# Performance work log

Measured on AMD Instinct MI355X. Metric: run time of the kernel, lower is better.

Reference implementation:

```python
import jax, jax.numpy as jnp
import numpy as np
from jax import lax

H = 512; MEL = 80; B = 8; S = 128; T = 200; NCH = 256


def _lstm_layer(x, Wih, Whh, bih, bhh, reverse=False):
    # x: [B, S, Din] -> [B, S, H]; PyTorch gate order i,f,g,o
    xs = jnp.swapaxes(x, 0, 1)
    bsz = x.shape[0]
    hid = Whh.shape[1]

    def step(carry, xt):
        h, c = carry
        g = xt @ Wih.T + bih + h @ Whh.T + bhh
        i, f, gg, o = jnp.split(g, 4, axis=-1)
        c2 = jax.nn.sigmoid(f) * c + jax.nn.sigmoid(i) * jnp.tanh(gg)
        h2 = jax.nn.sigmoid(o) * jnp.tanh(c2)
        return (h2, c2), h2

    init = (jnp.zeros((bsz, hid), x.dtype), jnp.zeros((bsz, hid), x.dtype))
    _, hs = lax.scan(step, init, xs, reverse=reverse)
    return jnp.swapaxes(hs, 0, 1)


def _forward(text_sequence, target_mel_len, emb, Wih00, Whh00, bih00, bhh00,
             Wih01, Whh01, bih01, bhh01, Wih10, Whh10, bih10, bhh10,
             Wih11, Whh11, bih11, bhh11, attn_W, attn_b, attn_v,
             dec_Wih, dec_Whh, dec_bih, dec_bhh, mel_W, mel_b):
    x = emb[text_sequence]  # [B,S,H] (dropout disabled: eval mode)
    f0 = _lstm_layer(x, Wih00, Whh00, bih00, bhh00)
    b0 = _lstm_layer(x, Wih01, Whh01, bih01, bhh01, reverse=True)
    x1 = jnp.concatenate([f0, b0], axis=-1)
    f1 = _lstm_layer(x1, Wih10, Whh10, bih10, bhh10)
    b1 = _lstm_layer(x1, Wih11, Whh11, bih11, bhh11, reverse=True)
    enc = jnp.concatenate([f1, b1], axis=-1)  # [B,S,2H]

    # attn Linear on cat(hidden, encoder): split weight into hidden/encoder parts
    W_h = attn_W[:, :H]
    W_e = attn_W[:, H:]
    enc_part = jnp.einsum('bsd,hd->bsh', enc, W_e) + attn_b  # hoisted out of loop
    bsz = text_sequence.shape[0]

    def step(carry, _):
        h, c, din = carry
        energy = jnp.tanh(enc_part + (h @ W_h.T)[:, None, :])  # [B,S,H]
        score = energy @ attn_v                                # [B,S]
        a = jax.nn.softmax(score, axis=1)
        ctx = jnp.einsum('bs,bsd->bd', a, enc)                 # [B,2H]
        xin = jnp.concatenate([din, ctx], axis=1)              # [B,MEL+2H]
        g = xin @ dec_Wih.T + dec_bih + h @ dec_Whh.T + dec_bhh
        i, f, gg, o = jnp.split(g, 4, axis=-1)
        c2 = jax.nn.sigmoid(f) * c + jax.nn.sigmoid(i) * jnp.tanh(gg)
        h2 = jax.nn.sigmoid(o) * jnp.tanh(c2)
        mel = h2 @ mel_W.T + mel_b                             # [B,MEL]
        return (h2, c2, mel), mel

    carry0 = (jnp.zeros((bsz, H), jnp.float32),
              jnp.zeros((bsz, H), jnp.float32),
              jnp.zeros((bsz, MEL), jnp.float32))
    _, mels = lax.scan(step, carry0, None, length=target_mel_len)
    return jnp.transpose(mels, (1, 2, 0))  # [B, MEL, T]


def setup_inputs() -> dict:
    key = jax.random.key(0)
    keys = jax.random.split(key, 64)
    ki = iter(range(64))

    def rn(shape, scale=0.05):
        return jax.random.normal(keys[next(ki)], shape, dtype=jnp.float32) * scale

    inp = {}
    inp['text_sequence'] = jax.random.randint(keys[next(ki)], (B, S), 0, NCH)
    inp['target_mel_len'] = T
    inp['emb'] = rn((NCH, H), 0.3)
    for l, din in ((0, H), (1, 2 * H)):
        for d in (0, 1):
            inp[f'Wih{l}{d}'] = rn((4 * H, din))
            inp[f'Whh{l}{d}'] = rn((4 * H, H))
            inp[f'bih{l}{d}'] = rn((4 * H,))
            inp[f'bhh{l}{d}'] = rn((4 * H,))
    inp['attn_W'] = rn((H, 3 * H))
    inp['attn_b'] = rn((H,))
    inp['attn_v'] = rn((H,))
    inp['dec_Wih'] = rn((4 * H, 2 * H + MEL))
    inp['dec_Whh'] = rn((4 * H, H))
    inp['dec_bih'] = rn((4 * H,))
    inp['dec_bhh'] = rn((4 * H,))
    inp['mel_W'] = rn((MEL, H))
    inp['mel_b'] = rn((MEL,))
    return inp


def reference(text_sequence, target_mel_len, emb, Wih00, Whh00, bih00, bhh00,
              Wih01, Whh01, bih01, bhh01, Wih10, Whh10, bih10, bhh10,
              Wih11, Whh11, bih11, bhh11, attn_W, attn_b, attn_v,
              dec_Wih, dec_Whh, dec_bih, dec_bhh, mel_W, mel_b):
    return _forward(text_sequence, target_mel_len, emb, Wih00, Whh00, bih00, bhh00,
                    Wih01, Whh01, bih01, bhh01, Wih10, Whh10, bih10, bhh10,
                    Wih11, Whh11, bih11, bhh11, attn_W, attn_b, attn_v,
                    dec_Wih, dec_Whh, dec_bih, dec_bhh, mel_W, mel_b)
```

## Files before the change

### kernel.cpp

```cpp
#include <hip/hip_runtime.h>

#define B_ 8
#define S_ 128
#define H_ 512
#define G_ 2048
#define MEL_ 80

#define FLG_DEC    0
#define FLG_L0     8192
#define FLG_L1     10240
#define OFF_H0S    12288
#define OFF_H1S    28672
#define OFF_DH     45056
#define OFF_ATT    53248
#define OFF_HW     54272
#define ZERO_WORDS 58368
#define OFF_X0     58368
#define OFF_GX0F   (OFF_X0 + 524288)
#define OFF_GX0B   (OFF_GX0F + 2097152)
#define OFF_H0     (OFF_GX0B + 2097152)
#define OFF_GX1F   (OFF_H0 + 1048576)
#define OFF_GX1B   (OFF_GX1F + 2097152)
#define OFF_ENC    (OFF_GX1B + 2097152)
#define OFF_ENCP   (OFF_ENC + 1048576)
#define OFF_WE     OFF_GX0F
#define OFF_WH2    OFF_GX0B
#define OFF_BA     (OFF_GX0B + 1048576)
#define OFF_BB     (OFF_GX0B + 1050624)

__device__ __forceinline__ float sigm_f(float x) {
    x = fminf(fmaxf(x, -30.f), 30.f);
    return 1.f / (1.f + __expf(-x));
}
__device__ __forceinline__ float tanh_f(float x) {
    x = fminf(fmaxf(x, -15.f), 15.f);
    float e = __expf(2.f * x);
    return (e - 1.f) / (e + 1.f);
}

__device__ __forceinline__ void agw_u(unsigned* p, unsigned v) {
    __hip_atomic_store(p, v, __ATOMIC_RELAXED, __HIP_MEMORY_SCOPE_AGENT);
}
__device__ __forceinline__ unsigned agr_u(const unsigned* p) {
    return __hip_atomic_load(p, __ATOMIC_RELAXED, __HIP_MEMORY_SCOPE_AGENT);
}
__device__ __forceinline__ void agw_f(float* p, float v) {
    agw_u((unsigned*)p, __float_as_uint(v));
}
__device__ __forceinline__ float agr_f(const float* p) {
    return __uint_as_float(agr_u((const unsigned*)p));
}

__device__ __forceinline__ float4 agr_f4(const float* p) {
    float4 v;
    asm volatile("global_load_dwordx4 %0, %1, off sc1\n\t"
                 "s_waitcnt vmcnt(0)"
                 : "=v"(v) : "v"(p) : "memory");
    return v;
}

__device__ __forceinline__ void poll_flags(const unsigned* flags, int nf, unsigned phase) {
    if ((int)threadIdx.x < nf) {
        while (agr_u(flags + threadIdx.x * 16) < phase)
            __builtin_amdgcn_s_sleep(1);
    }
    __syncthreads();
}

__device__ __forceinline__ void set_flag(unsigned* flag, unsigned phase) {
    asm volatile("s_waitcnt vmcnt(0) lgkmcnt(0)" ::: "memory");
    __syncthreads();
    if (threadIdx.x == 0)
        agw_u(flag, phase);
}

__global__ __launch_bounds__(256) void zero_kernel(float* p) {
    p[blockIdx.x * 256 + threadIdx.x] = 0.f;
}

__global__ __launch_bounds__(256) void embed_kernel(const int* __restrict__ text,
                                                    const float* __restrict__ emb,
                                                    float* __restrict__ X) {
    int i = blockIdx.x * 256 + threadIdx.x;
    int bs = i >> 7;
    int h4 = i & 127;
    int ch = text[bs];
    ((float4*)X)[i] = ((const float4*)emb)[ch * 128 + h4];
}

__global__ __launch_bounds__(256) void gemm_f32(const float* __restrict__ A, int lda,
                                                const float* __restrict__ W, int ldw,
                                                const float* __restrict__ b1,
                                                const float* __restrict__ b2,
                                                float* __restrict__ C, int ldc, int K) {
    __shared__ float As[32][68];
    __shared__ float Ws[32][68];
    int tid = threadIdx.x;
    int tx = tid & 15, ty = tid >> 4;
    int n0 = blockIdx.x * 64, m0 = blockIdx.y * 64;
    float acc[4][4] = {};
    int r  = tid >> 3;
    int c4 = (tid & 7) * 4;
    for (int k0 = 0; k0 < K; k0 += 32) {
        float4 a0 = *(const float4*)&A[(m0 + r) * lda + k0 + c4];
        float4 a1 = *(const float4*)&A[(m0 + r + 32) * lda + k0 + c4];
        float4 w0 = *(const float4*)&W[(n0 + r) * ldw + k0 + c4];
        float4 w1 = *(const float4*)&W[(n0 + r + 32) * ldw + k0 + c4];
        As[c4 + 0][r] = a0.x; As[c4 + 1][r] = a0.y; As[c4 + 2][r] = a0.z; As[c4 + 3][r] = a0.w;
        As[c4 + 0][r + 32] = a1.x; As[c4 + 1][r + 32] = a1.y; As[c4 + 2][r + 32] = a1.z; As[c4 + 3][r + 32] = a1.w;
        Ws[c4 + 0][r] = w0.x; Ws[c4 + 1][r] = w0.y; Ws[c4 + 2][r] = w0.z; Ws[c4 + 3][r] = w0.w;
        Ws[c4 + 0][r + 32] = w1.x; Ws[c4 + 1][r + 32] = w1.y; Ws[c4 + 2][r + 32] = w1.z; Ws[c4 + 3][r + 32] = w1.w;
        __syncthreads();
#pragma unroll 8
        for (int kk = 0; kk < 32; ++kk) {
            float4 av = *(const float4*)&As[kk][ty * 4];
            float4 wv = *(const float4*)&Ws[kk][tx * 4];
            acc[0][0] = fmaf(av.x, wv.x, acc[0][0]); acc[0][1] = fmaf(av.x, wv.y, acc[0][1]);
            acc[0][2] = fmaf(av.x, wv.z, acc[0][2]); acc[0][3] = fmaf(av.x, wv.w, acc[0][3]);
            acc[1][0] = fmaf(av.y, wv.x, acc[1][0]); acc[1][1] = fmaf(av.y, wv.y, acc[1][1]);
            acc[1][2] = fmaf(av.y, wv.z, acc[1][2]); acc[1][3] = fmaf(av.y, wv.w, acc[1][3]);
            acc[2][0] = fmaf(av.z, wv.x, acc[2][0]); acc[2][1] = fmaf(av.z, wv.y, acc[2][1]);
            acc[2][2] = fmaf(av.z, wv.z, acc[2][2]); acc[2][3] = fmaf(av.z, wv.w, acc[2][3]);
            acc[3][0] = fmaf(av.w, wv.x, acc[3][0]); acc[3][1] = fmaf(av.w, wv.y, acc[3][1]);
            acc[3][2] = fmaf(av.w, wv.z, acc[3][2]); acc[3][3] = fmaf(av.w, wv.w, acc[3][3]);
        }
        __syncthreads();
    }
#pragma unroll
    for (int i = 0; i < 4; ++i)
#pragma unroll
        for (int j = 0; j < 4; ++j) {
            int n = n0 + tx * 4 + j;
            int m = m0 + ty * 4 + i;
            float bias = (b1 ? b1[n] : 0.f) + (b2 ? b2[n] : 0.f);
            C[m * ldc + n] = acc[i][j] + bias;
        }
}

__global__ __launch_bounds__(256) void we_kernel(const float* __restrict__ Wih,
                                                 const float* __restrict__ ENC,
                                                 float* __restrict__ WE) {
    const float* A = Wih + 80;
    const float* W = ENC + (size_t)blockIdx.z * 131072;
    float* C = WE + (size_t)blockIdx.z * 262144;
    __shared__ float As[32][68];
    __shared__ float Ws[32][68];
    int tid = threadIdx.x;
    int tx = tid & 15, ty = tid >> 4;
    int n0 = blockIdx.x * 64, m0 = blockIdx.y * 64;
    float acc[4][4] = {};
    int r  = tid >> 3;
    int c4 = (tid & 7) * 4;
    for (int k0 = 0; k0 < 1024; k0 += 32) {
        float4 a0 = *(const float4*)&A[(size_t)(m0 + r) * 1104 + k0 + c4];
        float4 a1 = *(const float4*)&A[(size_t)(m0 + r + 32) * 1104 + k0 + c4];
        float4 w0 = *(const float4*)&W[(n0 + r) * 1024 + k0 + c4];
        float4 w1 = *(const float4*)&W[(n0 + r + 32) * 1024 + k0 + c4];
        As[c4 + 0][r] = a0.x; As[c4 + 1][r] = a0.y; As[c4 + 2][r] = a0.z; As[c4 + 3][r] = a0.w;
        As[c4 + 0][r + 32] = a1.x; As[c4 + 1][r + 32] = a1.y; As[c4 + 2][r + 32] = a1.z; As[c4 + 3][r + 32] = a1.w;
        Ws[c4 + 0][r] = w0.x; Ws[c4 + 1][r] = w0.y; Ws[c4 + 2][r] = w0.z; Ws[c4 + 3][r] = w0.w;
        Ws[c4 + 0][r + 32] = w1.x; Ws[c4 + 1][r + 32] = w1.y; Ws[c4 + 2][r + 32] = w1.z; Ws[c4 + 3][r + 32] = w1.w;
        __syncthreads();
#pragma unroll 8
        for (int kk = 0; kk < 32; ++kk) {
            float4 av = *(const float4*)&As[kk][ty * 4];
            float4 wv = *(const float4*)&Ws[kk][tx * 4];
            acc[0][0] = fmaf(av.x, wv.x, acc[0][0]); acc[0][1] = fmaf(av.x, wv.y, acc[0][1]);
            acc[0][2] = fmaf(av.x, wv.z, acc[0][2]); acc[0][3] = fmaf(av.x, wv.w, acc[0][3]);
            acc[1][0] = fmaf(av.y, wv.x, acc[1][0]); acc[1][1] = fmaf(av.y, wv.y, acc[1][1]);
            acc[1][2] = fmaf(av.y, wv.z, acc[1][2]); acc[1][3] = fmaf(av.y, wv.w, acc[1][3]);
            acc[2][0] = fmaf(av.z, wv.x, acc[2][0]); acc[2][1] = fmaf(av.z, wv.y, acc[2][1]);
            acc[2][2] = fmaf(av.z, wv.z, acc[2][2]); acc[2][3] = fmaf(av.z, wv.w, acc[2][3]);
            acc[3][0] = fmaf(av.w, wv.x, acc[3][0]); acc[3][1] = fmaf(av.w, wv.y, acc[3][1]);
            acc[3][2] = fmaf(av.w, wv.z, acc[3][2]); acc[3][3] = fmaf(av.w, wv.w, acc[3][3]);
        }
        __syncthreads();
    }
#pragma unroll
    for (int i = 0; i < 4; ++i)
#pragma unroll
        for (int j = 0; j < 4; ++j)
            C[(size_t)(m0 + ty * 4 + i) * 128 + n0 + tx * 4 + j] = acc[i][j];
}

__global__ __launch_bounds__(256) void wh2_kernel(const float* __restrict__ Wih,
                                                  const float* __restrict__ Whh,
                                                  const float* __restrict__ melW,
                                                  float* __restrict__ WH2) {
    int wg = blockIdx.x;
    int tid = threadIdx.x;
    int r = wg >> 1;
    int k = (wg & 1) * 256 + tid;
    __shared__ float wrow[80];
    if (tid < 80) wrow[tid] = Wih[(size_t)r * 1104 + tid];
    __syncthreads();
    float acc = Whh[(size_t)r * 512 + k];
#pragma unroll 8
    for (int m = 0; m < 80; ++m)
        acc = fmaf(wrow[m], melW[m * 512 + k], acc);
    WH2[(size_t)r * 512 + k] = acc;
}

__global__ __launch_bounds__(256) void bias_kernel(const float* __restrict__ Wih,
                                                   const float* __restrict__ bih,
                                                   const float* __restrict__ bhh,
                                                   const float* __restrict__ melb,
                                                   float* __restrict__ BA,
                                                   float* __restrict__ BB) {
    int r = blockIdx.x * 256 + threadIdx.x;
    float a = bih[r] + bhh[r];
    float b2 = 0.f;
#pragma unroll 8
    for (int m = 0; m < 80; ++m)
        b2 = fmaf(Wih[(size_t)r * 1104 + m], melb[m], b2);
    BA[r] = a;
    BB[r] = a + b2;
}

__global__ __launch_bounds__(256) void lstm_kernel(const float* __restrict__ GXf,
                                                   const float* __restrict__ GXb,
                                                   const float* __restrict__ Whh_f,
                                                   const float* __restrict__ Whh_b,
                                                   float* __restrict__ Hout,
                                                   float* __restrict__ hstate,
                                                   unsigned* __restrict__ flagsL) {
    int wg  = blockIdx.x;
    int s   = wg & 7;
    int g16 = wg >> 3;
    int dir = g16 >> 3;
    int b   = g16 & 7;
    const float* GX  = dir ? GXb : GXf;
    const float* Whh = dir ? Whh_b : Whh_f;
    float* hs = hstate + g16 * 1024;
    unsigned* fg = flagsL + g16 * 128;

    int tid = threadIdx.x;
    int g = tid >> 6, c = tid & 63;
    int col = s * 64 + c;
    int grow = g * 512 + col;
    const float* wr = Whh + (size_t)grow * 512;

    __shared__ float hsh[512];
    __shared__ float gvL[4][64];

    float cst = 0.f;

    for (int t = 0; t < 128; ++t) {
        poll_flags(fg, 8, (unsigned)t);
        if (tid < 128) {
            float4 v = agr_f4(hs + (t & 1) * 512 + tid * 4);
            *(float4*)&hsh[tid * 4] = v;
        }
        __syncthreads();

        int st = dir ? (127 - t) : t;
        float acc = GX[((size_t)b * S_ + st) * G_ + grow];
        float a0 = 0.f, a1 = 0.f, a2 = 0.f, a3 = 0.f;
#pragma unroll 8
        for (int k = 0; k < 512; k += 4) {
            float4 wv = *(const float4*)(wr + k);
            float4 hv = *(const float4*)&hsh[k];
            a0 = fmaf(wv.x, hv.x, a0); a1 = fmaf(wv.y, hv.y, a1);
            a2 = fmaf(wv.z, hv.z, a2); a3 = fmaf(wv.w, hv.w, a3);
        }
        gvL[g][c] = acc + (a0 + a1) + (a2 + a3);
        __syncthreads();

        float h2 = 0.f;
        if (tid < 64) {
            float gi = gvL[0][tid], gf = gvL[1][tid];
            float gg = gvL[2][tid], go = gvL[3][tid];
            float c2 = sigm_f(gf) * cst + sigm_f(gi) * tanh_f(gg);
            h2 = sigm_f(go) * tanh_f(c2);
            cst = c2;
            agw_f(hs + ((t & 1) ^ 1) * 512 + s * 64 + tid, h2);
        }
        set_flag(fg + s * 16, (unsigned)(t + 1));
        if (tid < 64)
            Hout[((size_t)b * S_ + st) * 1024 + dir * 512 + s * 64 + tid] = h2;
    }
}

__global__ __launch_bounds__(256) void decoder_kernel(float* __restrict__ ws,
                                                      const float* __restrict__ attn_W,
                                                      const float* __restrict__ attn_v,
                                                      const float* __restrict__ mel_W,
                                                      const float* __restrict__ mel_b,
                                                      float* __restrict__ out, int T,
                                                      unsigned* __restrict__ flags) {
    float* ENCP = ws + OFF_ENCP;
    float* DH   = ws + OFF_DH;
    float* ATT  = ws + OFF_ATT;
    float* HW   = ws + OFF_HW;
    const float* WE  = ws + OFF_WE;
    const float* WH2 = ws + OFF_WH2;
    const float* BA  = ws + OFF_BA;
    const float* BB  = ws + OFF_BB;

    int wg  = blockIdx.x;
    int tid = threadIdx.x;

    if (wg < 128) {
        int s = wg & 15;
        int b = wg >> 4;
        unsigned* fC = flags + b * 1024;
        unsigned* fA = fC + 16 * 16;
        unsigned* fB = fC + 32 * 16;

        int r   = tid >> 1;
        int half = tid & 1;
        int grow = (r >> 5) * 512 + s * 32 + (r & 31);
        const float* wh2_half = WH2 + (size_t)grow * 512 + half * 256;
        const float* we_row   = WE + ((size_t)b * 2048 + grow) * 128 + half * 64;
        float bias_a = (half == 0) ? BA[grow] : 0.f;
        float bias_b = (half == 0) ? BB[grow] : 0.f;
        int r2 = tid & 31, oct = tid >> 5;
        const float* wh_row = attn_W + (size_t)(s * 32 + r2) * 1536 + oct * 64;

        __shared__ float hsh[512];
        __shared__ float hwred[32][9];
        __shared__ float gBx[128][2];
        __shared__ float gv[128];
        __shared__ float attL[128];

        float cst = 0.f;

        for (int t = 0; t < T; ++t) {
            poll_flags(fC, 16, (unsigned)t);
            const float* DHr = DH + (t & 1) * 4096 + b * 512;
            if (tid < 128) {
                float4 v = agr_f4(DHr + tid * 4);
                *(float4*)&hsh[tid * 4] = v;
            }
            __syncthreads();
            {
                const float* hp = hsh + oct * 64;
                float w = 0.f;
#pragma unroll 8
                for (int k = 0; k < 64; k += 4) {
                    float4 wv = *(const float4*)(wh_row + k);
                    float4 hv = *(const float4*)(hp + k);
                    w = fmaf(wv.x, hv.x, w); w = fmaf(wv.y, hv.y, w);
                    w = fmaf(wv.z, hv.z, w); w = fmaf(wv.w, hv.w, w);
                }
                hwred[r2][oct] = w;
            }
            __syncthreads();
            if (tid < 32) {
                float hw = hwred[tid][0] + hwred[tid][1] + hwred[tid][2] + hwred[tid][3]
                         + hwred[tid][4] + hwred[tid][5] + hwred[tid][6] + hwred[tid][7];
                agw_f(HW + b * 512 + s * 32 + tid, hw);
            }
            set_flag(fA + s * 16, (unsigned)(t + 1));

            float wpart = (t == 0) ? bias_a : bias_b;
            {
                const float* hp = hsh + half * 256;
                float a0 = 0.f, a1 = 0.f, a2 = 0.f, a3 = 0.f;
#pragma unroll 8
                for (int k = 0; k < 256; k += 4) {
                    float4 wv = *(const float4*)(wh2_half + k);
                    float4 hv = *(const float4*)(hp + k);
                    a0 = fmaf(wv.x, hv.x, a0); a1 = fmaf(wv.y, hv.y, a1);
                    a2 = fmaf(wv.z, hv.z, a2); a3 = fmaf(wv.w, hv.w, a3);
                }
                wpart += (a0 + a1) + (a2 + a3);
            }

            poll_flags(fB, 1, (unsigned)(t + 1));
            if (tid < 32) {
                float4 v = agr_f4(ATT + b * 128 + tid * 4);
                *(float4*)&attL[tid * 4] = v;
            }
            __syncthreads();
            {
                const float* ap = attL + half * 64;
                float a0 = 0.f, a1 = 0.f, a2 = 0.f, a3 = 0.f;
#pragma unroll 8
                for (int k = 0; k < 64; k += 4) {
                    float4 wv = *(const float4*)(we_row + k);
                    a0 = fmaf(wv.x, ap[k + 0], a0); a1 = fmaf(wv.y, ap[k + 1], a1);
                    a2 = fmaf(wv.z, ap[k + 2], a2); a3 = fmaf(wv.w, ap[k + 3], a3);
                }
                gBx[r][half] = wpart + (a0 + a1) + (a2 + a3);
            }
            __syncthreads();
            if (tid < 128)
                gv[tid] = gBx[tid][0] + gBx[tid][1];
            __syncthreads();
            if (tid < 32) {
                float gi = gv[tid], gf = gv[32 + tid], gg = gv[64 + tid], go = gv[96 + tid];
                float c2 = sigm_f(gf) * cst + sigm_f(gi) * tanh_f(gg);
                float h2 = sigm_f(go) * tanh_f(c2);
                cst = c2;
                agw_f(DH + ((t + 1) & 1) * 4096 + b * 512 + s * 32 + tid, h2);
            }
            set_flag(fC + s * 16, (unsigned)(t + 1));
        }
    } else {
        int b = wg - 128;
        unsigned* fC = flags + b * 1024;
        unsigned* fA = fC + 16 * 16;
        unsigned* fB = fC + 32 * 16;

        __shared__ float hw2[512];
        __shared__ float dh2[512];
        __shared__ float scred[128][2];
        __shared__ float red[128];
        __shared__ float att[128];
        __shared__ float melp[80][2];

        int r = tid >> 1, half = tid & 1;

        for (int t = 0; t < T; ++t) {
            poll_flags(fA, 16, (unsigned)(t + 1));
            if (tid < 128) {
                float4 v = agr_f4(HW + b * 512 + tid * 4);
                *(float4*)&hw2[tid * 4] = v;
            }
            __syncthreads();

            {
                int sI = tid & 127, kh = tid >> 7;
                const float* ep = ENCP + ((size_t)b * S_ + sI) * 512 + kh * 256;
                const float* hp = hw2 + kh * 256;
                const float* vv = attn_v + kh * 256;
                float a0 = 0.f, a1 = 0.f, a2 = 0.f, a3 = 0.f;
#pragma unroll 4
                for (int k = 0; k < 256; k += 4) {
                    float4 e4 = *(const float4*)(ep + k);
                    float4 h4 = *(const float4*)(hp + k);
                    float4 v4 = *(const float4*)(vv + k);
                    a0 = fmaf(tanh_f(e4.x + h4.x), v4.x, a0);
                    a1 = fmaf(tanh_f(e4.y + h4.y), v4.y, a1);
                    a2 = fmaf(tanh_f(e4.z + h4.z), v4.z, a2);
                    a3 = fmaf(tanh_f(e4.w + h4.w), v4.w, a3);
                }
                scred[sI][kh] = (a0 + a1) + (a2 + a3);
            }
            __syncthreads();

            float sc = 0.f;
            if (tid < 128) {
                sc = scred[tid][0] + scred[tid][1];
                red[tid] = sc;
            }
            __syncthreads();
            for (int off = 64; off >= 1; off >>= 1) {
                if (tid < off) red[tid] = fmaxf(red[tid], red[tid + off]);
                __syncthreads();
            }
            float mx = red[0];
            __syncthreads();
            if (tid < 128) {
                float e = __expf(sc - mx);
                att[tid] = e;
                red[tid] = e;
            }
            __syncthreads();
            if (tid < 64) red[tid] += red[tid + 64];
            __syncthreads();
            for (int off = 32; off >= 1; off >>= 1) {
                if (tid < off) red[tid] += red[tid + off];
                __syncthreads();
            }
            float inv = 1.f / red[0];
            if (tid < 128)
                agw_f(ATT + b * 128 + tid, att[tid] * inv);
            set_flag(fB, (unsigned)(t + 1));

            if (t > 0) {
                if (tid < 128) {
                    float4 v = agr_f4(DH + (t & 1) * 4096 + b * 512 + tid * 4);
                    *(float4*)&dh2[tid * 4] = v;
                }
                __syncthreads();
                if (tid < 160) {
                    const float* wp = mel_W + (size_t)r * 512 + half * 256;
                    const float* hp = dh2 + half * 256;
                    float a0 = 0.f, a1 = 0.f, a2 = 0.f, a3 = 0.f;
#pragma unroll 8
                    for (int k = 0; k < 256; k += 4) {
                        float4 wv = *(const float4*)(wp + k);
                        float4 hv = *(const float4*)(hp + k);
                        a0 = fmaf(wv.x, hv.x, a0); a1 = fmaf(wv.y, hv.y, a1);
                        a2 = fmaf(wv.z, hv.z, a2); a3 = fmaf(wv.w, hv.w, a3);
                    }
                    melp[r][half] = (a0 + a1) + (a2 + a3);
                }
                __syncthreads();
                if (tid < 80)
                    out[b * MEL_ * T + tid * T + (t - 1)] = melp[tid][0] + melp[tid][1] + mel_b[tid];
            }
        }

        poll_flags(fC, 16, (unsigned)T);
        if (tid < 128) {
            float4 v = agr_f4(DH + (T & 1) * 4096 + b * 512 + tid * 4);
            *(float4*)&dh2[tid * 4] = v;
        }
        __syncthreads();
        if (tid < 160) {
            const float* wp = mel_W + (size_t)r * 512 + half * 256;
            const float* hp = dh2 + half * 256;
            float a0 = 0.f, a1 = 0.f, a2 = 0.f, a3 = 0.f;
#pragma unroll 8
            for (int k = 0; k < 256; k += 4) {
                float4 wv = *(const float4*)(wp + k);
                float4 hv = *(const float4*)(hp + k);
                a0 = fmaf(wv.x, hv.x, a0); a1 = fmaf(wv.y, hv.y, a1);
                a2 = fmaf(wv.z, hv.z, a2); a3 = fmaf(wv.w, hv.w, a3);
            }
            melp[r][half] = (a0 + a1) + (a2 + a3);
        }
        __syncthreads();
        if (tid < 80)
            out[b * MEL_ * T + tid * T + (T - 1)] = melp[tid][0] + melp[tid][1] + mel_b[tid];
    }
}

extern "C" void kernel_launch(void* const* d_in, const int* in_sizes, int n_in,
                              void* d_out, int out_size, void* d_ws, size_t ws_size,
                              hipStream_t stream) {
    const int*   text  = (const int*)d_in[0];
    const float* emb   = (const float*)d_in[2];
    const float* Wih00 = (const float*)d_in[3];
    const float* Whh00 = (const float*)d_in[4];
    const float* bih00 = (const float*)d_in[5];
    const float* bhh00 = (const float*)d_in[6];
    const float* Wih01 = (const float*)d_in[7];
    const float* Whh01 = (const float*)d_in[8];
    const float* bih01 = (const float*)d_in[9];
    const float* bhh01 = (const float*)d_in[10];
    const float* Wih10 = (const float*)d_in[11];
    const float* Whh10 = (const float*)d_in[12];
    const float* bih10 = (const float*)d_in[13];
    const float* bhh10 = (const float*)d_in[14];
    const float* Wih11 = (const float*)d_in[15];
    const float* Whh11 = (const float*)d_in[16];
    const float* bih11 = (const float*)d_in[17];
    const float* bhh11 = (const float*)d_in[18];
    const float* attn_W = (const float*)d_in[19];
    const float* attn_b = (const float*)d_in[20];
    const float* attn_v = (const float*)d_in[21];
    const float* dec_Wih = (const float*)d_in[22];
    const float* dec_Whh = (const float*)d_in[23];
    const float* dec_bih = (const float*)d_in[24];
    const float* dec_bhh = (const float*)d_in[25];
    const float* mel_W = (const float*)d_in[26];
    const float* mel_b = (const float*)d_in[27];

    float* ws = (float*)d_ws;
    unsigned* flags = (unsigned*)d_ws;
    float* out = (float*)d_out;
    int T = out_size / (B_ * MEL_);

    zero_kernel<<<ZERO_WORDS / 256, 256, 0, stream>>>(ws);

    embed_kernel<<<512, 256, 0, stream>>>(text, emb, ws + OFF_X0);

    gemm_f32<<<dim3(32, 16), 256, 0, stream>>>(ws + OFF_X0, 512, Wih00, 512,
                                               bih00, bhh00, ws + OFF_GX0F, 2048, 512);
    gemm_f32<<<dim3(32, 16), 256, 0, stream>>>(ws + OFF_X0, 512, Wih01, 512,
                                               bih01, bhh01, ws + OFF_GX0B, 2048, 512);
    lstm_kernel<<<128, 256, 0, stream>>>(ws + OFF_GX0F, ws + OFF_GX0B, Whh00, Whh01,
                                         ws + OFF_H0, ws + OFF_H0S, flags + FLG_L0);
    wh2_kernel<<<4096, 256, 0, stream>>>(dec_Wih, dec_Whh, mel_W, ws + OFF_WH2);
    bias_kernel<<<8, 256, 0, stream>>>(dec_Wih, dec_bih, dec_bhh, mel_b,
                                       ws + OFF_BA, ws + OFF_BB);
    gemm_f32<<<dim3(32, 16), 256, 0, stream>>>(ws + OFF_H0, 1024, Wih10, 1024,
                                               bih10, bhh10, ws + OFF_GX1F, 2048, 1024);
    gemm_f32<<<dim3(32, 16), 256, 0, stream>>>(ws + OFF_H0, 1024, Wih11, 1024,
                                               bih11, bhh11, ws + OFF_GX1B, 2048, 1024);
    lstm_kernel<<<128, 256, 0, stream>>>(ws + OFF_GX1F, ws + OFF_GX1B, Whh10, Whh11,
                                         ws + OFF_ENC, ws + OFF_H1S, flags + FLG_L1);
    gemm_f32<<<dim3(8, 16), 256, 0, stream>>>(ws + OFF_ENC, 1024, attn_W + 512, 1536,
                                              attn_b, nullptr, ws + OFF_ENCP, 512, 1024);
    we_kernel<<<dim3(2, 32, 8), 256, 0, stream>>>(dec_Wih, ws + OFF_ENC, ws + OFF_WE);
    decoder_kernel<<<136, 256, 0, stream>>>(ws, attn_W, attn_v, mel_W, mel_b, out, T,
                                            flags + FLG_DEC);
}
```

Baseline: 9.865 ms.

## Restructure decoder sync: move hidden-attention projection into attention block, fewer workgroups

The h@W_h projection moves out of the 128 gate workgroups and into the per-batch attention workgroup. This removes one cross-workgroup flag handshake (fA/HW) per decoder step. The gate workgroups drop from 128 to 64, each now computing a full 512-long dot product per gate row instead of two halves, with fewer reductions and barriers. Flag polling is also merged with the hidden-state loads in both the LSTM and decoder kernels, and only the writing wave waits before setting the flag, instead of a block-wide barrier. The trade-off is more serial work per step in the attention workgroup and less parallelism overall.

New measurement: 16.12 ms. +63.4%, slower.

```diff
diff --git a/kernel.cpp b/kernel.cpp
--- a/kernel.cpp
+++ b/kernel.cpp
@@ -47,9 +47,6 @@
 __device__ __forceinline__ void agw_f(float* p, float v) {
     agw_u((unsigned*)p, __float_as_uint(v));
 }
-__device__ __forceinline__ float agr_f(const float* p) {
-    return __uint_as_float(agr_u((const unsigned*)p));
-}
 
 __device__ __forceinline__ float4 agr_f4(const float* p) {
     float4 v;
@@ -57,21 +54,6 @@
                  "s_waitcnt vmcnt(0)"
                  : "=v"(v) : "v"(p) : "memory");
     return v;
-}
-
-__device__ __forceinline__ void poll_flags(const unsigned* flags, int nf, unsigned phase) {
-    if ((int)threadIdx.x < nf) {
-        while (agr_u(flags + threadIdx.x * 16) < phase)
-            __builtin_amdgcn_s_sleep(1);
-    }
-    __syncthreads();
-}
-
-__device__ __forceinline__ void set_flag(unsigned* flag, unsigned phase) {
-    asm volatile("s_waitcnt vmcnt(0) lgkmcnt(0)" ::: "memory");
-    __syncthreads();
-    if (threadIdx.x == 0)
-        agw_u(flag, phase);
 }
 
 __global__ __launch_bounds__(256) void zero_kernel(float* p) {
@@ -236,8 +218,7 @@
 
     int tid = threadIdx.x;
     int g = tid >> 6, c = tid & 63;
-    int col = s * 64 + c;
-    int grow = g * 512 + col;
+    int grow = g * 512 + s * 64 + c;
     const float* wr = Whh + (size_t)grow * 512;
 
     __shared__ float hsh[512];
@@ -246,10 +227,11 @@
     float cst = 0.f;
 
     for (int t = 0; t < 128; ++t) {
-        poll_flags(fg, 8, (unsigned)t);
         if (tid < 128) {
-            float4 v = agr_f4(hs + (t & 1) * 512 + tid * 4);
-            *(float4*)&hsh[tid * 4] = v;
+            const unsigned* f = fg + (tid >> 4) * 16;
+            while (agr_u(f) < (unsigned)t)
+                __builtin_amdgcn_s_sleep(1);
+            *(float4*)&hsh[tid * 4] = agr_f4(hs + (t & 1) * 512 + tid * 4);
         }
         __syncthreads();
 
@@ -266,18 +248,18 @@
         gvL[g][c] = acc + (a0 + a1) + (a2 + a3);
         __syncthreads();
 
-        float h2 = 0.f;
         if (tid < 64) {
             float gi = gvL[0][tid], gf = gvL[1][tid];
             float gg = gvL[2][tid], go = gvL[3][tid];
             float c2 = sigm_f(gf) * cst + sigm_f(gi) * tanh_f(gg);
-            h2 = sigm_f(go) * tanh_f(c2);
+            float h2 = sigm_f(go) * tanh_f(c2);
             cst = c2;
             agw_f(hs + ((t & 1) ^ 1) * 512 + s * 64 + tid, h2);
-        }
-        set_flag(fg + s * 16, (unsigned)(t + 1));
-        if (tid < 64)
+            asm volatile("s_waitcnt vmcnt(0)" ::: "memory");
+            if (tid == 0)
+                agw_u(fg + s * 16, (unsigned)(t + 1));
             Hout[((size_t)b * S_ + st) * 1024 + dir * 512 + s * 64 + tid] = h2;
+        }
     }
 }
 
@@ -291,7 +273,6 @@
     float* ENCP = ws + OFF_ENCP;
     float* DH   = ws + OFF_DH;
     float* ATT  = ws + OFF_ATT;
-    float* HW   = ws + OFF_HW;
     const float* WE  = ws + OFF_WE;
     const float* WH2 = ws + OFF_WH2;
     const float* BA  = ws + OFF_BA;
@@ -300,111 +281,85 @@
     int wg  = blockIdx.x;
     int tid = threadIdx.x;
 
-    if (wg < 128) {
-        int s = wg & 15;
-        int b = wg >> 4;
+    if (wg < 64) {
+        int s = wg & 7;
+        int b = wg >> 3;
         unsigned* fC = flags + b * 1024;
-        unsigned* fA = fC + 16 * 16;
-        unsigned* fB = fC + 32 * 16;
-
-        int r   = tid >> 1;
-        int half = tid & 1;
-        int grow = (r >> 5) * 512 + s * 32 + (r & 31);
-        const float* wh2_half = WH2 + (size_t)grow * 512 + half * 256;
-        const float* we_row   = WE + ((size_t)b * 2048 + grow) * 128 + half * 64;
-        float bias_a = (half == 0) ? BA[grow] : 0.f;
-        float bias_b = (half == 0) ? BB[grow] : 0.f;
-        int r2 = tid & 31, oct = tid >> 5;
-        const float* wh_row = attn_W + (size_t)(s * 32 + r2) * 1536 + oct * 64;
+        unsigned* fB = fC + 8 * 16;
+
+        int g = tid >> 6, c = tid & 63;
+        int grow = g * 512 + s * 64 + c;
+        const float* wh2_row = WH2 + (size_t)grow * 512;
+        const float* we_row  = WE + ((size_t)b * 2048 + grow) * 128;
+        float bias_a = BA[grow];
+        float bias_b = BB[grow];
 
         __shared__ float hsh[512];
-        __shared__ float hwred[32][9];
-        __shared__ float gBx[128][2];
-        __shared__ float gv[128];
         __shared__ float attL[128];
+        __shared__ float gvL[4][64];
 
         float cst = 0.f;
 
         for (int t = 0; t < T; ++t) {
-            poll_flags(fC, 16, (unsigned)t);
-            const float* DHr = DH + (t & 1) * 4096 + b * 512;
             if (tid < 128) {
-                float4 v = agr_f4(DHr + tid * 4);
-                *(float4*)&hsh[tid * 4] = v;
-            }
-            __syncthreads();
-            {
-                const float* hp = hsh + oct * 64;
-                float w = 0.f;
-#pragma unroll 8
-                for (int k = 0; k < 64; k += 4) {
-                    float4 wv = *(const float4*)(wh_row + k);
-                    float4 hv = *(const float4*)(hp + k);
-                    w = fmaf(wv.x, hv.x, w); w = fmaf(wv.y, hv.y, w);
-                    w = fmaf(wv.z, hv.z, w); w = fmaf(wv.w, hv.w, w);
-                }
-                hwred[r2][oct] = w;
-            }
-            __syncthreads();
-            if (tid < 32) {
-                float hw = hwred[tid][0] + hwred[tid][1] + hwred[tid][2] + hwred[tid][3]
-                         + hwred[tid][4] + hwred[tid][5] + hwred[tid][6] + hwred[tid][7];
-                agw_f(HW + b * 512 + s * 32 + tid, hw);
-            }
-            set_flag(fA + s * 16, (unsigned)(t + 1));
+                const unsigned* f = fC + (tid >> 4) * 16;
+                while (agr_u(f) < (unsigned)t)
+                    __builtin_amdgcn_s_sleep(1);
+                *(float4*)&hsh[tid * 4] = agr_f4(DH + (t & 1) * 4096 + b * 512 + tid * 4);
+            }
+            __syncthreads();
 
             float wpart = (t == 0) ? bias_a : bias_b;
             {
-                const float* hp = hsh + half * 256;
                 float a0 = 0.f, a1 = 0.f, a2 = 0.f, a3 = 0.f;
 #pragma unroll 8
-                for (int k = 0; k < 256; k += 4) {
-                    float4 wv = *(const float4*)(wh2_half + k);
-                    float4 hv = *(const float4*)(hp + k);
+                for (int k = 0; k < 512; k += 4) {
+                    float4 wv = *(const float4*)(wh2_row + k);
+                    float4 hv = *(const float4*)&hsh[k];
                     a0 = fmaf(wv.x, hv.x, a0); a1 = fmaf(wv.y, hv.y, a1);
                     a2 = fmaf(wv.z, hv.z, a2); a3 = fmaf(wv.w, hv.w, a3);
                 }
                 wpart += (a0 + a1) + (a2 + a3);
             }
 
-            poll_flags(fB, 1, (unsigned)(t + 1));
             if (tid < 32) {
-                float4 v = agr_f4(ATT + b * 128 + tid * 4);
-                *(float4*)&attL[tid * 4] = v;
-            }
-            __syncthreads();
+                while (agr_u(fB) < (unsigned)(t + 1))
+                    __builtin_amdgcn_s_sleep(1);
+                *(float4*)&attL[tid * 4] = agr_f4(ATT + b * 128 + tid * 4);
+            }
+            __syncthreads();
+
             {
-                const float* ap = attL + half * 64;
                 float a0 = 0.f, a1 = 0.f, a2 = 0.f, a3 = 0.f;
 #pragma unroll 8
-                for (int k = 0; k < 64; k += 4) {
+                for (int k = 0; k < 128; k += 4) {
                     float4 wv = *(const float4*)(we_row + k);
-                    a0 = fmaf(wv.x, ap[k + 0], a0); a1 = fmaf(wv.y, ap[k + 1], a1);
-                    a2 = fmaf(wv.z, ap[k + 2], a2); a3 = fmaf(wv.w, ap[k + 3], a3);
+                    a0 = fmaf(wv.x, attL[k + 0], a0); a1 = fmaf(wv.y, attL[k + 1], a1);
+                    a2 = fmaf(wv.z, attL[k + 2], a2); a3 = fmaf(wv.w, attL[k + 3], a3);
                 }
-                gBx[r][half] = wpart + (a0 + a1) + (a2 + a3);
-            }
-            __syncthreads();
-            if (tid < 128)
-                gv[tid] = gBx[tid][0] + gBx[tid][1];
-            __syncthreads();
-            if (tid < 32) {
-                float gi = gv[tid], gf = gv[32 + tid], gg = gv[64 + tid], go = gv[96 + tid];
+                gvL[g][c] = wpart + (a0 + a1) + (a2 + a3);
+            }
+            __syncthreads();
+
+            if (tid < 64) {
+                float gi = gvL[0][tid], gf = gvL[1][tid];
+                float gg = gvL[2][tid], go = gvL[3][tid];
                 float c2 = sigm_f(gf) * cst + sigm_f(gi) * tanh_f(gg);
                 float h2 = sigm_f(go) * tanh_f(c2);
                 cst = c2;
-                agw_f(DH + ((t + 1) & 1) * 4096 + b * 512 + s * 32 + tid, h2);
-            }
-            set_flag(fC + s * 16, (unsigned)(t + 1));
+                agw_f(DH + ((t + 1) & 1) * 4096 + b * 512 + s * 64 + tid, h2);
+                asm volatile("s_waitcnt vmcnt(0)" ::: "memory");
+                if (tid == 0)
+                    agw_u(fC + s * 16, (unsigned)(t + 1));
+            }
         }
     } else {
-        int b = wg - 128;
+        int b = wg - 64;
         unsigned* fC = flags + b * 1024;
-        unsigned* fA = fC + 16 * 16;
-        unsigned* fB = fC + 32 * 16;
-
-        __shared__ float hw2[512];
+        unsigned* fB = fC + 8 * 16;
+
         __shared__ float dh2[512];
+        __shared__ float hw[512];
         __shared__ float scred[128][2];
         __shared__ float red[128];
         __shared__ float att[128];
@@ -413,17 +368,34 @@
         int r = tid >> 1, half = tid & 1;
 
         for (int t = 0; t < T; ++t) {
-            poll_flags(fA, 16, (unsigned)(t + 1));
             if (tid < 128) {
-                float4 v = agr_f4(HW + b * 512 + tid * 4);
-                *(float4*)&hw2[tid * 4] = v;
+                const unsigned* f = fC + (tid >> 4) * 16;
+                while (agr_u(f) < (unsigned)t)
+                    __builtin_amdgcn_s_sleep(1);
+                *(float4*)&dh2[tid * 4] = agr_f4(DH + (t & 1) * 4096 + b * 512 + tid * 4);
+            }
+            __syncthreads();
+
+#pragma unroll
+            for (int rr = 0; rr < 2; ++rr) {
+                int row = tid + rr * 256;
+                const float* wr = attn_W + (size_t)row * 1536;
+                float a0 = 0.f, a1 = 0.f, a2 = 0.f, a3 = 0.f;
+#pragma unroll 8
+                for (int k = 0; k < 512; k += 4) {
+                    float4 wv = *(const float4*)(wr + k);
+                    float4 hv = *(const float4*)&dh2[k];
+                    a0 = fmaf(wv.x, hv.x, a0); a1 = fmaf(wv.y, hv.y, a1);
+                    a2 = fmaf(wv.z, hv.z, a2); a3 = fmaf(wv.w, hv.w, a3);
+                }
+                hw[row] = (a0 + a1) + (a2 + a3);
             }
             __syncthreads();
 
             {
                 int sI = tid & 127, kh = tid >> 7;
                 const float* ep = ENCP + ((size_t)b * S_ + sI) * 512 + kh * 256;
-                const float* hp = hw2 + kh * 256;
+                const float* hp = hw + kh * 256;
                 const float* vv = attn_v + kh * 256;
                 float a0 = 0.f, a1 = 0.f, a2 = 0.f, a3 = 0.f;
 #pragma unroll 4
@@ -465,16 +437,18 @@
                 __syncthreads();
             }
             float inv = 1.f / red[0];
-            if (tid < 128)
-                agw_f(ATT + b * 128 + tid, att[tid] * inv);
-            set_flag(fB, (unsigned)(t + 1));
+
+            if (tid < 32) {
+                agw_f(ATT + b * 128 + tid * 4 + 0, att[tid * 4 + 0] * inv);
+                agw_f(ATT + b * 128 + tid * 4 + 1, att[tid * 4 + 1] * inv);
+                agw_f(ATT + b * 128 + tid * 4 + 2, att[tid * 4 + 2] * inv);
+                agw_f(ATT + b * 128 + tid * 4 + 3, att[tid * 4 + 3] * inv);
+                asm volatile("s_waitcnt vmcnt(0)" ::: "memory");
+                if (tid == 0)
+                    agw_u(fB, (unsigned)(t + 1));
+            }
 
             if (t > 0) {
-                if (tid < 128) {
-                    float4 v = agr_f4(DH + (t & 1) * 4096 + b * 512 + tid * 4);
-                    *(float4*)&dh2[tid * 4] = v;
-                }
-                __syncthreads();
                 if (tid < 160) {
                     const float* wp = mel_W + (size_t)r * 512 + half * 256;
                     const float* hp = dh2 + half * 256;
@@ -491,13 +465,16 @@
                 __syncthreads();
                 if (tid < 80)
                     out[b * MEL_ * T + tid * T + (t - 1)] = melp[tid][0] + melp[tid][1] + mel_b[tid];
-            }
-        }
-
-        poll_flags(fC, 16, (unsigned)T);
+            } else {
+                __syncthreads();
+            }
+        }
+
         if (tid < 128) {
-            float4 v = agr_f4(DH + (T & 1) * 4096 + b * 512 + tid * 4);
-            *(float4*)&dh2[tid * 4] = v;
+            const unsigned* f = fC + (tid >> 4) * 16;
+            while (agr_u(f) < (unsigned)T)
+                __builtin_amdgcn_s_sleep(1);
+            *(float4*)&dh2[tid * 4] = agr_f4(DH + (T & 1) * 4096 + b * 512 + tid * 4);
         }
         __syncthreads();
         if (tid < 160) {
@@ -577,6 +554,6 @@
     gemm_f32<<<dim3(8, 16), 256, 0, stream>>>(ws + OFF_ENC, 1024, attn_W + 512, 1536,
                                               attn_b, nullptr, ws + OFF_ENCP, 512, 1024);
     we_kernel<<<dim3(2, 32, 8), 256, 0, stream>>>(dec_Wih, ws + OFF_ENC, ws + OFF_WE);
-    decoder_kernel<<<136, 256, 0, stream>>>(ws, attn_W, attn_v, mel_W, mel_b, out, T,
-                                            flags + FLG_DEC);
-}
+    decoder_kernel<<<72, 256, 0, stream>>>(ws, attn_W, attn_v, mel_W, mel_b, out, T,
+                                           flags + FLG_DEC);
+}
```

## Replace block-wide flag polling with per-slice waits and wavefront-local flag release

Applied to the files above, without the earlier changes.

Each loader thread now waits only on the flag of the producer block that wrote its slice of the hidden state, instead of a few threads polling every flag followed by a block barrier. Flags are released from inside the single producing wavefront after its own stores drain, dropping the extra __syncthreads per phase. Together these shorten the per-step handoff latency in the LSTM and decoder recurrences. The ordering now depends on vmcnt waits within one wavefront plus relaxed agent-scope atomics, which is subtle to get right.

New measurement: 9.927 ms. Within noise of the previous version (+0.6%).

```diff
diff --git a/kernel.cpp b/kernel.cpp
--- a/kernel.cpp
+++ b/kernel.cpp
@@ -47,9 +47,6 @@
 __device__ __forceinline__ void agw_f(float* p, float v) {
     agw_u((unsigned*)p, __float_as_uint(v));
 }
-__device__ __forceinline__ float agr_f(const float* p) {
-    return __uint_as_float(agr_u((const unsigned*)p));
-}
 
 __device__ __forceinline__ float4 agr_f4(const float* p) {
     float4 v;
@@ -57,21 +54,6 @@
                  "s_waitcnt vmcnt(0)"
                  : "=v"(v) : "v"(p) : "memory");
     return v;
-}
-
-__device__ __forceinline__ void poll_flags(const unsigned* flags, int nf, unsigned phase) {
-    if ((int)threadIdx.x < nf) {
-        while (agr_u(flags + threadIdx.x * 16) < phase)
-            __builtin_amdgcn_s_sleep(1);
-    }
-    __syncthreads();
-}
-
-__device__ __forceinline__ void set_flag(unsigned* flag, unsigned phase) {
-    asm volatile("s_waitcnt vmcnt(0) lgkmcnt(0)" ::: "memory");
-    __syncthreads();
-    if (threadIdx.x == 0)
-        agw_u(flag, phase);
 }
 
 __global__ __launch_bounds__(256) void zero_kernel(float* p) {
@@ -236,8 +218,7 @@
 
     int tid = threadIdx.x;
     int g = tid >> 6, c = tid & 63;
-    int col = s * 64 + c;
-    int grow = g * 512 + col;
+    int grow = g * 512 + s * 64 + c;
     const float* wr = Whh + (size_t)grow * 512;
 
     __shared__ float hsh[512];
@@ -246,10 +227,11 @@
     float cst = 0.f;
 
     for (int t = 0; t < 128; ++t) {
-        poll_flags(fg, 8, (unsigned)t);
         if (tid < 128) {
-            float4 v = agr_f4(hs + (t & 1) * 512 + tid * 4);
-            *(float4*)&hsh[tid * 4] = v;
+            const unsigned* f = fg + (tid >> 4) * 16;
+            while (agr_u(f) < (unsigned)t)
+                __builtin_amdgcn_s_sleep(1);
+            *(float4*)&hsh[tid * 4] = agr_f4(hs + (t & 1) * 512 + tid * 4);
         }
         __syncthreads();
 
@@ -266,18 +248,18 @@
         gvL[g][c] = acc + (a0 + a1) + (a2 + a3);
         __syncthreads();
 
-        float h2 = 0.f;
         if (tid < 64) {
             float gi = gvL[0][tid], gf = gvL[1][tid];
             float gg = gvL[2][tid], go = gvL[3][tid];
             float c2 = sigm_f(gf) * cst + sigm_f(gi) * tanh_f(gg);
-            h2 = sigm_f(go) * tanh_f(c2);
+            float h2 = sigm_f(go) * tanh_f(c2);
             cst = c2;
             agw_f(hs + ((t & 1) ^ 1) * 512 + s * 64 + tid, h2);
-        }
-        set_flag(fg + s * 16, (unsigned)(t + 1));
-        if (tid < 64)
+            asm volatile("s_waitcnt vmcnt(0)" ::: "memory");
+            if (tid == 0)
+                agw_u(fg + s * 16, (unsigned)(t + 1));
             Hout[((size_t)b * S_ + st) * 1024 + dir * 512 + s * 64 + tid] = h2;
+        }
     }
 }
 
@@ -326,13 +308,14 @@
         float cst = 0.f;
 
         for (int t = 0; t < T; ++t) {
-            poll_flags(fC, 16, (unsigned)t);
-            const float* DHr = DH + (t & 1) * 4096 + b * 512;
             if (tid < 128) {
-                float4 v = agr_f4(DHr + tid * 4);
-                *(float4*)&hsh[tid * 4] = v;
-            }
-            __syncthreads();
+                const unsigned* f = fC + (tid >> 3) * 16;
+                while (agr_u(f) < (unsigned)t)
+                    __builtin_amdgcn_s_sleep(1);
+                *(float4*)&hsh[tid * 4] = agr_f4(DH + (t & 1) * 4096 + b * 512 + tid * 4);
+            }
+            __syncthreads();
+
             {
                 const float* hp = hsh + oct * 64;
                 float w = 0.f;
@@ -350,8 +333,10 @@
                 float hw = hwred[tid][0] + hwred[tid][1] + hwred[tid][2] + hwred[tid][3]
                          + hwred[tid][4] + hwred[tid][5] + hwred[tid][6] + hwred[tid][7];
                 agw_f(HW + b * 512 + s * 32 + tid, hw);
-            }
-            set_flag(fA + s * 16, (unsigned)(t + 1));
+                asm volatile("s_waitcnt vmcnt(0)" ::: "memory");
+                if (tid == 0)
+                    agw_u(fA + s * 16, (unsigned)(t + 1));
+            }
 
             float wpart = (t == 0) ? bias_a : bias_b;
             {
@@ -367,12 +352,13 @@
                 wpart += (a0 + a1) + (a2 + a3);
             }
 
-            poll_flags(fB, 1, (unsigned)(t + 1));
             if (tid < 32) {
-                float4 v = agr_f4(ATT + b * 128 + tid * 4);
-                *(float4*)&attL[tid * 4] = v;
-            }
-            __syncthreads();
+                while (agr_u(fB) < (unsigned)(t + 1))
+                    __builtin_amdgcn_s_sleep(1);
+                *(float4*)&attL[tid * 4] = agr_f4(ATT + b * 128 + tid * 4);
+            }
+            __syncthreads();
+
             {
                 const float* ap = attL + half * 64;
                 float a0 = 0.f, a1 = 0.f, a2 = 0.f, a3 = 0.f;
@@ -394,8 +380,10 @@
                 float h2 = sigm_f(go) * tanh_f(c2);
                 cst = c2;
                 agw_f(DH + ((t + 1) & 1) * 4096 + b * 512 + s * 32 + tid, h2);
-            }
-            set_flag(fC + s * 16, (unsigned)(t + 1));
+                asm volatile("s_waitcnt vmcnt(0)" ::: "memory");
+                if (tid == 0)
+                    agw_u(fC + s * 16, (unsigned)(t + 1));
+            }
         }
     } else {
         int b = wg - 128;
@@ -413,10 +401,11 @@
         int r = tid >> 1, half = tid & 1;
 
         for (int t = 0; t < T; ++t) {
-            poll_flags(fA, 16, (unsigned)(t + 1));
             if (tid < 128) {
-                float4 v = agr_f4(HW + b * 512 + tid * 4);
-                *(float4*)&hw2[tid * 4] = v;
+                const unsigned* f = fA + (tid >> 3) * 16;
+                while (agr_u(f) < (unsigned)(t + 1))
+                    __builtin_amdgcn_s_sleep(1);
+                *(float4*)&hw2[tid * 4] = agr_f4(HW + b * 512 + tid * 4);
             }
             __syncthreads();
 
@@ -465,14 +454,23 @@
                 __syncthreads();
             }
             float inv = 1.f / red[0];
-            if (tid < 128)
-                agw_f(ATT + b * 128 + tid, att[tid] * inv);
-            set_flag(fB, (unsigned)(t + 1));
+
+            if (tid < 32) {
+                agw_f(ATT + b * 128 + tid * 4 + 0, att[tid * 4 + 0] * inv);
+                agw_f(ATT + b * 128 + tid * 4 + 1, att[tid * 4 + 1] * inv);
+                agw_f(ATT + b * 128 + tid * 4 + 2, att[tid * 4 + 2] * inv);
+                agw_f(ATT + b * 128 + tid * 4 + 3, att[tid * 4 + 3] * inv);
+                asm volatile("s_waitcnt vmcnt(0)" ::: "memory");
+                if (tid == 0)
+                    agw_u(fB, (unsigned)(t + 1));
+            }
 
             if (t > 0) {
                 if (tid < 128) {
-                    float4 v = agr_f4(DH + (t & 1) * 4096 + b * 512 + tid * 4);
-                    *(float4*)&dh2[tid * 4] = v;
+                    const unsigned* f = fC + (tid >> 3) * 16;
+                    while (agr_u(f) < (unsigned)t)
+                        __builtin_amdgcn_s_sleep(1);
+                    *(float4*)&dh2[tid * 4] = agr_f4(DH + (t & 1) * 4096 + b * 512 + tid * 4);
                 }
                 __syncthreads();
                 if (tid < 160) {
@@ -494,10 +492,11 @@
             }
         }
 
-        poll_flags(fC, 16, (unsigned)T);
         if (tid < 128) {
-            float4 v = agr_f4(DH + (T & 1) * 4096 + b * 512 + tid * 4);
-            *(float4*)&dh2[tid * 4] = v;
+            const unsigned* f = fC + (tid >> 3) * 16;
+            while (agr_u(f) < (unsigned)T)
+                __builtin_amdgcn_s_sleep(1);
+            *(float4*)&dh2[tid * 4] = agr_f4(DH + (T & 1) * 4096 + b * 512 + tid * 4);
         }
         __syncthreads();
         if (tid < 160) {
```
